# Kernel tuning notes

Measured on AMD Instinct MI355X. Metric: run time of the kernel, lower is better.

The kernel has to match this reference:

```python
import jax, jax.numpy as jnp
import numpy as np
import math

B, L, D, H = 2, 2048, 1024, 16
HD = D // H  # 64
SYNC_THRESHOLD = -0.7
LN_EPS = 1e-12


def setup_inputs() -> dict:
    key = jax.random.key(0)
    ks = jax.random.split(key, 12)
    s = 0.02
    return {
        "hidden_states": jax.random.normal(ks[0], (B, L, D), dtype=jnp.float32),
        "attention_mask": jnp.zeros((B, 1, 1, L), dtype=jnp.float32),
        "phi": jax.random.normal(ks[1], (B, L, H), dtype=jnp.float32),
        "Wq": jax.random.normal(ks[2], (D, D), dtype=jnp.float32) * s,
        "bq": jnp.zeros((D,), dtype=jnp.float32),
        "Wk": jax.random.normal(ks[3], (D, D), dtype=jnp.float32) * s,
        "bk": jnp.zeros((D,), dtype=jnp.float32),
        "Wv": jax.random.normal(ks[4], (D, D), dtype=jnp.float32) * s,
        "bv": jnp.zeros((D,), dtype=jnp.float32),
        "Wo": jax.random.normal(ks[5], (D, D), dtype=jnp.float32) * s,
        "bo": jnp.zeros((D,), dtype=jnp.float32),
        "ln_g": jnp.ones((D,), dtype=jnp.float32),
        "ln_b": jnp.zeros((D,), dtype=jnp.float32),
    }


def _shape(x):  # [B,L,D] -> [B,H,L,HD]
    return x.reshape(B, L, H, HD).transpose(0, 2, 1, 3)


def _rotate_half(x):
    x1, x2 = jnp.split(x, 2, axis=-1)
    return jnp.concatenate([-x2, x1], axis=-1)


def reference(hidden_states, attention_mask, phi, Wq, bq, Wk, bk, Wv, bv, Wo, bo, ln_g, ln_b):
    residual = hidden_states
    q = _shape(hidden_states @ Wq.T + bq)
    k = _shape(hidden_states @ Wk.T + bk)
    v = _shape(hidden_states @ Wv.T + bv)

    # phase per (batch, head, token): [B,H,L,1]; constant across head_dim,
    # so cos/sin of the concatenated phase are the same scalar per token/head.
    p = jnp.transpose(phi, (0, 2, 1))[..., None]
    cos_p = jnp.cos(p)
    sin_p = jnp.sin(p)
    q_rot = q * cos_p + _rotate_half(q) * sin_p
    k_rot = k * cos_p + _rotate_half(k) * sin_p

    scores = jnp.einsum("bhqd,bhkd->bhqk", q_rot, k_rot) / math.sqrt(HD)

    # data-dependent sync mask: mask pairs whose phase difference is anti-synced
    delta_phi = p - jnp.swapaxes(p, -1, -2)           # [B,H,L,L]
    eye = jnp.eye(L, dtype=bool)[None, None]          # [1,1,L,L]
    sync_mask = (jnp.cos(delta_phi) < SYNC_THRESHOLD) & ~eye
    scores = jnp.where(sync_mask, -1e9, scores)
    scores = scores + attention_mask

    # all-masked edge case: zero diagonal score so softmax attends to self
    row_max = jnp.max(scores, axis=-1, keepdims=True)
    all_masked = row_max <= -1e8
    scores = jnp.where(all_masked & eye, 0.0, scores)

    probs = jax.nn.softmax(scores, axis=-1)
    ctx = jnp.einsum("bhqk,bhkd->bhqd", probs, v)
    ctx = ctx.transpose(0, 2, 1, 3).reshape(B, L, D)

    out = ctx @ Wo.T + bo
    x = out + residual
    mean = jnp.mean(x, axis=-1, keepdims=True)
    var = jnp.var(x, axis=-1, keepdims=True)
    return (x - mean) / jnp.sqrt(var + LN_EPS) * ln_g + ln_b
```

## Files before the change

### kernel.cpp

```cpp
#include <hip/hip_runtime.h>
#include <cmath>

#define BB 2
#define LL 2048
#define DD 1024
#define HH 16
#define HDD 64

typedef _Float16 v8h __attribute__((ext_vector_type(8)));
typedef _Float16 v4h __attribute__((ext_vector_type(4)));
typedef _Float16 v2h __attribute__((ext_vector_type(2)));
typedef float v4f __attribute__((ext_vector_type(4)));

#define LOG2E 1.44269504089f
#define NEGB  (-1.442695e9f)

#define GLD(gp, lp)                                                        \
  __builtin_amdgcn_global_load_lds(                                        \
      (const __attribute__((address_space(1))) void*)(gp),                 \
      (__attribute__((address_space(3))) void*)(lp), 16, 0, 0)

__global__ __launch_bounds__(256) void prep(
    const float* __restrict__ hs, const float* __restrict__ wq,
    const float* __restrict__ wk, const float* __restrict__ wv,
    const float* __restrict__ wo, const float* __restrict__ phi,
    const float* __restrict__ amk, _Float16* __restrict__ hsh,
    _Float16* __restrict__ wqkvh, _Float16* __restrict__ woh,
    unsigned* __restrict__ csh2, float* __restrict__ aml2)
{
  const int i = blockIdx.x * 256 + threadIdx.x;
  if (i < 2097152) {
    const float* s;
    _Float16* d;
    if (i < 1048576)      { s = hs + (size_t)i * 4;            d = hsh + (size_t)i * 4; }
    else if (i < 1310720) { int j = i - 1048576; s = wq + (size_t)j * 4; d = wqkvh + (size_t)j * 4; }
    else if (i < 1572864) { int j = i - 1310720; s = wk + (size_t)j * 4; d = wqkvh + 1048576 + (size_t)j * 4; }
    else if (i < 1835008) { int j = i - 1572864; s = wv + (size_t)j * 4; d = wqkvh + 2097152 + (size_t)j * 4; }
    else                  { int j = i - 1835008; s = wo + (size_t)j * 4; d = woh + (size_t)j * 4; }
    float4 v = *(const float4*)s;
    v4h o;
    o[0] = (_Float16)v.x; o[1] = (_Float16)v.y;
    o[2] = (_Float16)v.z; o[3] = (_Float16)v.w;
    *(v4h*)d = o;
  } else {
    const int o = i - 2097152;
    if (o < BB * LL) aml2[o] = amk[o] * LOG2E;
    const int l = o & 2047;
    const int h = (o >> 11) & 15;
    const int b = o >> 15;
    const float ph = phi[(b * 2048 + l) * 16 + h];
    v2h cs;
    cs[0] = (_Float16)cosf(ph);
    cs[1] = (_Float16)sinf(ph);
    csh2[o] = __builtin_bit_cast(unsigned, cs);
  }
}

__device__ __forceinline__ void gemm_loop(
    const _Float16* __restrict__ A, const _Float16* __restrict__ W, const int K,
    const int m0, const int n0, const int tid, const int wave, const int lane,
    _Float16* As, _Float16* Bs, v4f acc[4][4])
{
  const int quad = lane >> 4;
  const int ql = lane & 15;
  const int wm = (wave >> 1) * 64;
  const int wn = (wave & 1) * 64;
  const int srow = tid >> 2;
  const int skof = (tid & 3) * 8;
  const _Float16* Ap = A + (size_t)(m0 + srow) * K + skof;
  const _Float16* Wp = W + (size_t)(n0 + srow) * K + skof;
  const size_t rstep = (size_t)64 * K;
  for (int k0 = 0; k0 < K; k0 += 32) {
    __syncthreads();
    GLD(Ap + k0,         As + tid * 8);
    GLD(Ap + rstep + k0, As + 2048 + tid * 8);
    GLD(Wp + k0,         Bs + tid * 8);
    GLD(Wp + rstep + k0, Bs + 2048 + tid * 8);
    __syncthreads();
    v8h af[4], bf[4];
#pragma unroll
    for (int mt = 0; mt < 4; ++mt)
      af[mt] = *(const v8h*)&As[(wm + mt * 16 + ql) * 32 + quad * 8];
#pragma unroll
    for (int nt = 0; nt < 4; ++nt)
      bf[nt] = *(const v8h*)&Bs[(wn + nt * 16 + ql) * 32 + quad * 8];
#pragma unroll
    for (int mt = 0; mt < 4; ++mt)
#pragma unroll
      for (int nt = 0; nt < 4; ++nt)
        acc[mt][nt] = __builtin_amdgcn_mfma_f32_16x16x32_f16(
            af[mt], bf[nt], acc[mt][nt], 0, 0, 0);
  }
}

__global__ __launch_bounds__(256) void gemm_qkv(
    const _Float16* __restrict__ A, const _Float16* __restrict__ W,
    const float* __restrict__ bqp, const float* __restrict__ bkp,
    const float* __restrict__ bvp, const unsigned* __restrict__ csh2,
    _Float16* __restrict__ qh, _Float16* __restrict__ kh,
    _Float16* __restrict__ vt2)
{
  __shared__ _Float16 As[128 * 32];
  __shared__ _Float16 Bs[128 * 32];
  const int tid = threadIdx.x, lane = tid & 63, wave = tid >> 6;
  const int quad = lane >> 4, ql = lane & 15;
  const int bid0 = blockIdx.y * 24 + blockIdx.x;
  const int bid  = (bid0 & 7) * 96 + (bid0 >> 3);
  const int m0 = (bid / 24) * 128, n0 = (bid % 24) * 128;
  v4f acc[4][4];
#pragma unroll
  for (int mt = 0; mt < 4; ++mt)
#pragma unroll
    for (int nt = 0; nt < 4; ++nt) acc[mt][nt] = (v4f){0.f, 0.f, 0.f, 0.f};
  gemm_loop(A, W, DD, m0, n0, tid, wave, lane, As, Bs, acc);

  const int buf = n0 >> 10;
  const int col0 = (n0 & 1023) + (wave & 1) * 64;
  const int hh = col0 >> 6;
  const int mr0 = m0 + (wave >> 1) * 64;

  if (buf == 2) {
    float bb4[4];
#pragma unroll
    for (int nt = 0; nt < 4; ++nt) bb4[nt] = bvp[col0 + nt * 16 + ql];
#pragma unroll
    for (int mt = 0; mt < 4; ++mt) {
      const int row = mr0 + mt * 16 + quad * 4;
      const int b_ = row >> 11;
      const int l = row & 2047;
      _Float16* dst = vt2 + ((size_t)(b_ * 16 + hh) * 32 + (l >> 6)) * 4096 +
                      ((l >> 2) & 15) * 256;
#pragma unroll
      for (int nt = 0; nt < 4; ++nt) {
        const int d = nt * 16 + ql;
        v4h o4;
#pragma unroll
        for (int r = 0; r < 4; ++r) o4[r] = (_Float16)(acc[mt][nt][r] + bb4[nt]);
        *(v4h*)&dst[d * 4] = o4;
      }
    }
  } else {
    const float scl = (buf == 0) ? 0.125f * LOG2E : 1.0f;
    _Float16* outp = (buf == 0) ? qh : kh;
    const float* bias = (buf == 0) ? bqp : bkp;
    float bb4[4];
#pragma unroll
    for (int nt = 0; nt < 4; ++nt) bb4[nt] = bias[col0 + nt * 16 + ql];
#pragma unroll
    for (int mt = 0; mt < 4; ++mt)
#pragma unroll
      for (int r = 0; r < 4; ++r) {
        const int row = mr0 + mt * 16 + quad * 4 + r;
        const int b_ = row >> 11;
        const int l = row & 2047;
        const v2h c2 = __builtin_bit_cast(
            v2h, csh2[(b_ * 16 + hh) * 2048 + l]);
        const float c = (float)c2[0], s = (float)c2[1];
        _Float16* orow = outp + (size_t)row * DD + col0 + ql;
#pragma unroll
        for (int pp = 0; pp < 2; ++pp) {
          const float a0 = acc[mt][pp][r] + bb4[pp];
          const float a1 = acc[mt][pp + 2][r] + bb4[pp + 2];
          orow[pp * 16]        = (_Float16)((a0 * c - a1 * s) * scl);
          orow[(pp + 2) * 16]  = (_Float16)((a1 * c + a0 * s) * scl);
        }
      }
  }
}

__global__ __launch_bounds__(256) void gemm_o(
    const _Float16* __restrict__ A, const _Float16* __restrict__ W,
    const float* __restrict__ bo, const float* __restrict__ res,
    float* __restrict__ out)
{
  __shared__ _Float16 As[128 * 32];
  __shared__ _Float16 Bs[64 * 32];
  const int tid = threadIdx.x, lane = tid & 63, wave = tid >> 6;
  const int quad = lane >> 4, ql = lane & 15;
  const int bid0 = blockIdx.y * 16 + blockIdx.x;
  const int bid  = (bid0 & 7) * 64 + (bid0 >> 3);
  const int m0 = (bid / 16) * 128, n0 = (bid % 16) * 64;
  v4f acc[4][2];
#pragma unroll
  for (int mt = 0; mt < 4; ++mt)
#pragma unroll
    for (int nt = 0; nt < 2; ++nt) acc[mt][nt] = (v4f){0.f, 0.f, 0.f, 0.f};
  const int wm = (wave >> 1) * 64;
  const int wn = (wave & 1) * 32;
  const int srow = tid >> 2;
  const int skof = (tid & 3) * 8;
  const _Float16* Ap = A + (size_t)(m0 + srow) * DD + skof;
  const _Float16* Wp = W + (size_t)(n0 + srow) * DD + skof;
  const size_t rstep = (size_t)64 * DD;
  for (int k0 = 0; k0 < DD; k0 += 32) {
    __syncthreads();
    GLD(Ap + k0,         As + tid * 8);
    GLD(Ap + rstep + k0, As + 2048 + tid * 8);
    GLD(Wp + k0,         Bs + tid * 8);
    __syncthreads();
    v8h af[4], bf[2];
#pragma unroll
    for (int mt = 0; mt < 4; ++mt)
      af[mt] = *(const v8h*)&As[(wm + mt * 16 + ql) * 32 + quad * 8];
#pragma unroll
    for (int nt = 0; nt < 2; ++nt)
      bf[nt] = *(const v8h*)&Bs[(wn + nt * 16 + ql) * 32 + quad * 8];
#pragma unroll
    for (int mt = 0; mt < 4; ++mt)
#pragma unroll
      for (int nt = 0; nt < 2; ++nt)
        acc[mt][nt] = __builtin_amdgcn_mfma_f32_16x16x32_f16(
            af[mt], bf[nt], acc[mt][nt], 0, 0, 0);
  }
#pragma unroll
  for (int nt = 0; nt < 2; ++nt) {
    const int col = n0 + wn + nt * 16 + ql;
    const float bb = bo[col];
#pragma unroll
    for (int mt = 0; mt < 4; ++mt)
#pragma unroll
      for (int r = 0; r < 4; ++r) {
        const int row = m0 + wm + mt * 16 + quad * 4 + r;
        const size_t ix = (size_t)row * DD + col;
        out[ix] = acc[mt][nt][r] + bb + res[ix];
      }
  }
}

__global__ __launch_bounds__(256, 2) void attn_db(
    const _Float16* __restrict__ Q, const _Float16* __restrict__ K,
    const _Float16* __restrict__ VT2, const unsigned* __restrict__ csh2,
    const float* __restrict__ aml2, _Float16* __restrict__ ctx)
{
  __shared__ _Float16 Kt[2][4096];
  __shared__ _Float16 Vt[2][4096];
  __shared__ float amL[LL];

  const int tid  = threadIdx.x;
  const int lane = tid & 63;
  const int wave = tid >> 6;
  const int quad = lane >> 4;
  const int ql   = lane & 15;
  const int bid  = blockIdx.x;
  const int bh = bid & 31;
  const int qt = bid >> 5;
  const int h  = bh & 15;
  const int b  = bh >> 4;
  const int q0w = qt * 128 + wave * 32;
  const int csb = bh * LL;

  {
    const float* amb = aml2 + b * LL;
    for (int i = tid; i < LL; i += 256) amL[i] = amb[i];
  }

  v8h qf0[2], qf1[2];
  v4h bq0, bq1;
  {
    const _Float16* qp = Q + ((size_t)(b * LL + q0w + ql)) * DD + h * 64 + quad * 8;
    qf0[0] = *(const v8h*)qp;
    qf0[1] = *(const v8h*)(qp + 32);
    const v2h c2 = __builtin_bit_cast(v2h, csh2[csb + q0w + ql]);
    v4h t = (v4h){0, 0, 0, 0};
    if (quad == 0) { t[0] = c2[0]; t[1] = c2[1]; }
    bq0 = t;
  }
  {
    const _Float16* qp = Q + ((size_t)(b * LL + q0w + 16 + ql)) * DD + h * 64 + quad * 8;
    qf1[0] = *(const v8h*)qp;
    qf1[1] = *(const v8h*)(qp + 32);
    const v2h c2 = __builtin_bit_cast(v2h, csh2[csb + q0w + 16 + ql]);
    v4h t = (v4h){0, 0, 0, 0};
    if (quad == 0) { t[0] = c2[0]; t[1] = c2[1]; }
    bq1 = t;
  }
  const v4h ones = (v4h){(_Float16)1.f, (_Float16)1.f,
                         (_Float16)1.f, (_Float16)1.f};

  v4f o0[4], o1[4];
#pragma unroll
  for (int nt = 0; nt < 4; ++nt) {
    o0[nt] = (v4f){0.f, 0.f, 0.f, 0.f};
    o1[nt] = (v4f){0.f, 0.f, 0.f, 0.f};
  }
  v4f lacc0 = (v4f){0.f, 0.f, 0.f, 0.f};
  v4f lacc1 = (v4f){0.f, 0.f, 0.f, 0.f};

  const _Float16* Kb   = K + (size_t)(b * LL) * DD + h * 64;
  const _Float16* VTb2 = VT2 + (size_t)bh * 131072;
  const unsigned* csk = csh2 + csb;

  const int srow = tid >> 3;
  const int kch  = (tid & 7) ^ (srow & 7);

  {
    const size_t kg = (size_t)srow * 1024 + kch * 8;
    GLD(Kb + kg,             &Kt[0][tid * 8]);
    GLD(Kb + kg + 32 * 1024, &Kt[0][2048 + tid * 8]);
    GLD(VTb2 + tid * 8,          &Vt[0][tid * 8]);
    GLD(VTb2 + 2048 + tid * 8,   &Vt[0][2048 + tid * 8]);
  }
  unsigned cs_cur[4], cs_nxt[4];
#pragma unroll
  for (int c = 0; c < 4; ++c) cs_cur[c] = csk[c * 16 + ql];
  __syncthreads();

  for (int tt = 0; tt < 16; ++tt) {
#pragma unroll
    for (int u = 0; u < 2; ++u) {
      const int t = tt * 2 + u;
      const int k0 = t * 64;
      if (t < 31) {
        const int k1 = k0 + 64;
        const size_t kg = (size_t)(k1 + srow) * 1024 + kch * 8;
        GLD(Kb + kg,             &Kt[u ^ 1][tid * 8]);
        GLD(Kb + kg + 32 * 1024, &Kt[u ^ 1][2048 + tid * 8]);
        const _Float16* vsrc = VTb2 + (size_t)(t + 1) * 4096;
        GLD(vsrc + tid * 8,        &Vt[u ^ 1][tid * 8]);
        GLD(vsrc + 2048 + tid * 8, &Vt[u ^ 1][2048 + tid * 8]);
#pragma unroll
        for (int c = 0; c < 4; ++c) cs_nxt[c] = csk[k1 + c * 16 + ql];
      }
      const _Float16* KtB = Kt[u];
      const _Float16* VtB = Vt[u];

      v4f st0[4], st1[4], dd0[4], dd1[4];
#pragma unroll
      for (int c = 0; c < 4; ++c) {
        const int row = c * 16 + ql;
        const int sw = row & 7;
        v8h a0 = *(const v8h*)&KtB[row * 64 + ((quad ^ sw) << 3)];
        v8h a1 = *(const v8h*)&KtB[row * 64 + (((quad + 4) ^ sw) << 3)];
        v4f z0 = (v4f){0.f, 0.f, 0.f, 0.f};
        z0 = __builtin_amdgcn_mfma_f32_16x16x32_f16(a0, qf0[0], z0, 0, 0, 0);
        z0 = __builtin_amdgcn_mfma_f32_16x16x32_f16(a1, qf0[1], z0, 0, 0, 0);
        st0[c] = z0;
        v4f z1 = (v4f){0.f, 0.f, 0.f, 0.f};
        z1 = __builtin_amdgcn_mfma_f32_16x16x32_f16(a0, qf1[0], z1, 0, 0, 0);
        z1 = __builtin_amdgcn_mfma_f32_16x16x32_f16(a1, qf1[1], z1, 0, 0, 0);
        st1[c] = z1;
        const v2h c2 = __builtin_bit_cast(v2h, cs_cur[c]);
        v4h a = (v4h){0, 0, 0, 0};
        if (quad == 0) { a[0] = c2[0]; a[1] = c2[1]; }
        dd0[c] = __builtin_amdgcn_mfma_f32_16x16x16f16(
            a, bq0, (v4f){0.f, 0.f, 0.f, 0.f}, 0, 0, 0);
        dd1[c] = __builtin_amdgcn_mfma_f32_16x16x16f16(
            a, bq1, (v4f){0.f, 0.f, 0.f, 0.f}, 0, 0, 0);
      }

      v4h pf0[4], pf1[4];
#pragma unroll
      for (int c = 0; c < 4; ++c) {
        const v4f am4 = *(const v4f*)&amL[k0 + c * 16 + quad * 4];
        float p0[4], p1[4];
#pragma unroll
        for (int r = 0; r < 4; ++r) {
          p0[r] = __builtin_amdgcn_exp2f(
              ((dd0[c][r] < -0.7f) ? NEGB : st0[c][r]) + am4[r]);
          p1[r] = __builtin_amdgcn_exp2f(
              ((dd1[c][r] < -0.7f) ? NEGB : st1[c][r]) + am4[r]);
        }
        const unsigned a01 = __builtin_bit_cast(
            unsigned, __builtin_amdgcn_cvt_pkrtz(p0[0], p0[1]));
        const unsigned a23 = __builtin_bit_cast(
            unsigned, __builtin_amdgcn_cvt_pkrtz(p0[2], p0[3]));
        pf0[c] = __builtin_bit_cast(v4h, make_uint2(a01, a23));
        const unsigned b01 = __builtin_bit_cast(
            unsigned, __builtin_amdgcn_cvt_pkrtz(p1[0], p1[1]));
        const unsigned b23 = __builtin_bit_cast(
            unsigned, __builtin_amdgcn_cvt_pkrtz(p1[2], p1[3]));
        pf1[c] = __builtin_bit_cast(v4h, make_uint2(b01, b23));
      }

      __builtin_amdgcn_s_setprio(1);
#pragma unroll
      for (int c = 0; c < 4; ++c) {
        lacc0 = __builtin_amdgcn_mfma_f32_16x16x16f16(pf0[c], ones, lacc0, 0, 0, 0);
        lacc1 = __builtin_amdgcn_mfma_f32_16x16x16f16(pf1[c], ones, lacc1, 0, 0, 0);
#pragma unroll
        for (int nt = 0; nt < 4; ++nt) {
          const v4h vv = *(const v4h*)&VtB[((c * 4 + quad) * 64 +
                                            nt * 16 + ql) * 4];
          o0[nt] = __builtin_amdgcn_mfma_f32_16x16x16f16(pf0[c], vv, o0[nt], 0, 0, 0);
          o1[nt] = __builtin_amdgcn_mfma_f32_16x16x16f16(pf1[c], vv, o1[nt], 0, 0, 0);
        }
      }
      __builtin_amdgcn_s_setprio(0);
#pragma unroll
      for (int c = 0; c < 4; ++c) cs_cur[c] = cs_nxt[c];
      __syncthreads();
    }
  }

#pragma unroll
  for (int g = 0; g < 2; ++g) {
    const v4f* op = g ? o1 : o0;
    const v4f la = g ? lacc1 : lacc0;
#pragma unroll
    for (int r = 0; r < 4; ++r) {
      const int q = q0w + g * 16 + quad * 4 + r;
      const float lr = la[r];
      const size_t ob = (size_t)(b * LL + q) * DD + h * 64 + ql;
      if (lr <= 0.f) {
        const _Float16* vsrc = VTb2 + (q >> 6) * 4096 +
                               ((q >> 2) & 15) * 256 + (q & 3);
#pragma unroll
        for (int nt = 0; nt < 4; ++nt)
          ctx[ob + nt * 16] = vsrc[(nt * 16 + ql) * 4];
      } else {
        const float inv = 1.f / lr;
        ctx[ob + 0]  = (_Float16)(op[0][r] * inv);
        ctx[ob + 16] = (_Float16)(op[1][r] * inv);
        ctx[ob + 32] = (_Float16)(op[2][r] * inv);
        ctx[ob + 48] = (_Float16)(op[3][r] * inv);
      }
    }
  }
}

__global__ __launch_bounds__(256) void layernorm(
    const float* __restrict__ x, const float* __restrict__ g,
    const float* __restrict__ bta, float* __restrict__ out)
{
  __shared__ float red[8];
  const int row = blockIdx.x;
  const int tid = threadIdx.x;
  const float4 vv = ((const float4*)(x + (size_t)row * DD))[tid];
  float lsum = vv.x + vv.y + vv.z + vv.w;
  float lsq  = vv.x * vv.x + vv.y * vv.y + vv.z * vv.z + vv.w * vv.w;
#pragma unroll
  for (int off = 32; off > 0; off >>= 1) {
    lsum += __shfl_down(lsum, off, 64);
    lsq  += __shfl_down(lsq,  off, 64);
  }
  const int wid = tid >> 6;
  if ((tid & 63) == 0) { red[wid] = lsum; red[wid + 4] = lsq; }
  __syncthreads();
  const float tsum = red[0] + red[1] + red[2] + red[3];
  const float tsq  = red[4] + red[5] + red[6] + red[7];
  const float mean = tsum * (1.f / DD);
  const float var  = tsq * (1.f / DD) - mean * mean;
  const float inv  = rsqrtf(var + 1e-12f);
  const float4 gg = ((const float4*)g)[tid];
  const float4 bb = ((const float4*)bta)[tid];
  float4 oo;
  oo.x = (vv.x - mean) * inv * gg.x + bb.x;
  oo.y = (vv.y - mean) * inv * gg.y + bb.y;
  oo.z = (vv.z - mean) * inv * gg.z + bb.z;
  oo.w = (vv.w - mean) * inv * gg.w + bb.w;
  ((float4*)(out + (size_t)row * DD))[tid] = oo;
}

extern "C" void kernel_launch(void* const* d_in, const int* in_sizes, int n_in,
                              void* d_out, int out_size, void* d_ws, size_t ws_size,
                              hipStream_t stream)
{
  const float* hs  = (const float*)d_in[0];
  const float* amk = (const float*)d_in[1];
  const float* phi = (const float*)d_in[2];
  const float* Wq  = (const float*)d_in[3];
  const float* bq  = (const float*)d_in[4];
  const float* Wk  = (const float*)d_in[5];
  const float* bk  = (const float*)d_in[6];
  const float* Wv  = (const float*)d_in[7];
  const float* bv  = (const float*)d_in[8];
  const float* Wo  = (const float*)d_in[9];
  const float* bo  = (const float*)d_in[10];
  const float* lng = (const float*)d_in[11];
  const float* lnb = (const float*)d_in[12];
  float* out = (float*)d_out;

  const size_t SZ = (size_t)BB * LL * DD;
  _Float16* hsh   = (_Float16*)d_ws;
  _Float16* qh    = hsh + SZ;
  _Float16* kh    = qh + SZ;
  _Float16* vt2   = kh + SZ;
  _Float16* ctxh  = vt2 + SZ;
  _Float16* wqkvh = ctxh + SZ;
  _Float16* woh   = wqkvh + 3 * (size_t)DD * DD;
  float* xb    = (float*)(woh + (size_t)DD * DD);
  unsigned* csh2 = (unsigned*)(xb + SZ);
  float* aml2 = (float*)(csh2 + (size_t)BB * HH * LL);

  prep<<<8448, 256, 0, stream>>>(hs, Wq, Wk, Wv, Wo, phi, amk,
                                 hsh, wqkvh, woh, csh2, aml2);
  gemm_qkv<<<dim3(24, 32), 256, 0, stream>>>(hsh, wqkvh, bq, bk, bv, csh2,
                                             qh, kh, vt2);
  attn_db<<<512, 256, 0, stream>>>(qh, kh, vt2, csh2, aml2, ctxh);
  gemm_o<<<dim3(16, 32), 256, 0, stream>>>(ctxh, woh, bo, hs, xb);
  layernorm<<<BB * LL, 256, 0, stream>>>(xb, lng, lnb, out);
}
```

Before: 230.7 us.

## Fuse output projection with LayerNorm via atomic row stats and grid sync

Merges the output GEMM and the LayerNorm kernel into one cooperative kernel. Each block adds bias and residual in registers, then atomically accumulates per-row sum and sum-of-squares into global buffers that prep zeroes. After a grid-wide sync it normalizes in place and writes the final output. This removes the fp32 intermediate round trip and one kernel launch, at the cost of a grid barrier, atomic contention, and the requirement that all 512 blocks be co-resident.

After: 348.4 us. +51.0%, slower.

```diff
diff --git a/kernel.cpp b/kernel.cpp
--- a/kernel.cpp
+++ b/kernel.cpp
@@ -1,5 +1,8 @@
 #include <hip/hip_runtime.h>
+#include <hip/hip_cooperative_groups.h>
 #include <cmath>
+
+namespace cg = cooperative_groups;
 
 #define BB 2
 #define LL 2048
@@ -26,7 +29,8 @@
     const float* __restrict__ wo, const float* __restrict__ phi,
     const float* __restrict__ amk, _Float16* __restrict__ hsh,
     _Float16* __restrict__ wqkvh, _Float16* __restrict__ woh,
-    unsigned* __restrict__ csh2, float* __restrict__ aml2)
+    unsigned* __restrict__ csh2, float* __restrict__ aml2,
+    float* __restrict__ rsum, float* __restrict__ rsq)
 {
   const int i = blockIdx.x * 256 + threadIdx.x;
   if (i < 2097152) {
@@ -42,7 +46,7 @@
     o[0] = (_Float16)v.x; o[1] = (_Float16)v.y;
     o[2] = (_Float16)v.z; o[3] = (_Float16)v.w;
     *(v4h*)d = o;
-  } else {
+  } else if (i < 2162688) {
     const int o = i - 2097152;
     if (o < BB * LL) aml2[o] = amk[o] * LOG2E;
     const int l = o & 2047;
@@ -53,6 +57,10 @@
     cs[0] = (_Float16)cosf(ph);
     cs[1] = (_Float16)sinf(ph);
     csh2[o] = __builtin_bit_cast(unsigned, cs);
+  } else {
+    const int z = i - 2162688;
+    rsum[z] = 0.f;
+    rsq[z]  = 0.f;
   }
 }
 
@@ -168,9 +176,11 @@
   }
 }
 
-__global__ __launch_bounds__(256) void gemm_o(
+__global__ __launch_bounds__(256, 2) void gemm_o_ln(
     const _Float16* __restrict__ A, const _Float16* __restrict__ W,
     const float* __restrict__ bo, const float* __restrict__ res,
+    const float* __restrict__ g, const float* __restrict__ bta,
+    float* __restrict__ rsum, float* __restrict__ rsq,
     float* __restrict__ out)
 {
   __shared__ _Float16 As[128 * 32];
@@ -212,19 +222,61 @@
         acc[mt][nt] = __builtin_amdgcn_mfma_f32_16x16x32_f16(
             af[mt], bf[nt], acc[mt][nt], 0, 0, 0);
   }
-#pragma unroll
-  for (int nt = 0; nt < 2; ++nt) {
-    const int col = n0 + wn + nt * 16 + ql;
-    const float bb = bo[col];
-#pragma unroll
-    for (int mt = 0; mt < 4; ++mt)
-#pragma unroll
-      for (int r = 0; r < 4; ++r) {
+
+  float bb[2];
+#pragma unroll
+  for (int nt = 0; nt < 2; ++nt) bb[nt] = bo[n0 + wn + nt * 16 + ql];
+#pragma unroll
+  for (int mt = 0; mt < 4; ++mt)
+#pragma unroll
+    for (int r = 0; r < 4; ++r) {
+      const int row = m0 + wm + mt * 16 + quad * 4 + r;
+#pragma unroll
+      for (int nt = 0; nt < 2; ++nt) {
+        const int col = n0 + wn + nt * 16 + ql;
+        acc[mt][nt][r] += bb[nt] + res[(size_t)row * DD + col];
+      }
+    }
+#pragma unroll
+  for (int mt = 0; mt < 4; ++mt)
+#pragma unroll
+    for (int r = 0; r < 4; ++r) {
+      const float a = acc[mt][0][r], b = acc[mt][1][r];
+      float s = a + b;
+      float q2 = a * a + b * b;
+#pragma unroll
+      for (int off = 1; off < 16; off <<= 1) {
+        s  += __shfl_xor(s,  off, 64);
+        q2 += __shfl_xor(q2, off, 64);
+      }
+      if (ql == 0) {
         const int row = m0 + wm + mt * 16 + quad * 4 + r;
-        const size_t ix = (size_t)row * DD + col;
-        out[ix] = acc[mt][nt][r] + bb + res[ix];
-      }
-  }
+        atomicAdd(&rsum[row], s);
+        atomicAdd(&rsq[row],  q2);
+      }
+    }
+  __threadfence();
+  cg::this_grid().sync();
+
+#pragma unroll
+  for (int mt = 0; mt < 4; ++mt)
+#pragma unroll
+    for (int r = 0; r < 4; ++r) {
+      const int row = m0 + wm + mt * 16 + quad * 4 + r;
+      const float ts = __hip_atomic_load(&rsum[row], __ATOMIC_RELAXED,
+                                         __HIP_MEMORY_SCOPE_AGENT);
+      const float tq = __hip_atomic_load(&rsq[row], __ATOMIC_RELAXED,
+                                         __HIP_MEMORY_SCOPE_AGENT);
+      const float mean = ts * (1.f / DD);
+      const float var  = tq * (1.f / DD) - mean * mean;
+      const float inv  = rsqrtf(var + 1e-12f);
+#pragma unroll
+      for (int nt = 0; nt < 2; ++nt) {
+        const int col = n0 + wn + nt * 16 + ql;
+        out[(size_t)row * DD + col] =
+            (acc[mt][nt][r] - mean) * inv * g[col] + bta[col];
+      }
+    }
 }
 
 __global__ __launch_bounds__(256, 2) void attn_db(
@@ -418,39 +470,6 @@
   }
 }
 
-__global__ __launch_bounds__(256) void layernorm(
-    const float* __restrict__ x, const float* __restrict__ g,
-    const float* __restrict__ bta, float* __restrict__ out)
-{
-  __shared__ float red[8];
-  const int row = blockIdx.x;
-  const int tid = threadIdx.x;
-  const float4 vv = ((const float4*)(x + (size_t)row * DD))[tid];
-  float lsum = vv.x + vv.y + vv.z + vv.w;
-  float lsq  = vv.x * vv.x + vv.y * vv.y + vv.z * vv.z + vv.w * vv.w;
-#pragma unroll
-  for (int off = 32; off > 0; off >>= 1) {
-    lsum += __shfl_down(lsum, off, 64);
-    lsq  += __shfl_down(lsq,  off, 64);
-  }
-  const int wid = tid >> 6;
-  if ((tid & 63) == 0) { red[wid] = lsum; red[wid + 4] = lsq; }
-  __syncthreads();
-  const float tsum = red[0] + red[1] + red[2] + red[3];
-  const float tsq  = red[4] + red[5] + red[6] + red[7];
-  const float mean = tsum * (1.f / DD);
-  const float var  = tsq * (1.f / DD) - mean * mean;
-  const float inv  = rsqrtf(var + 1e-12f);
-  const float4 gg = ((const float4*)g)[tid];
-  const float4 bb = ((const float4*)bta)[tid];
-  float4 oo;
-  oo.x = (vv.x - mean) * inv * gg.x + bb.x;
-  oo.y = (vv.y - mean) * inv * gg.y + bb.y;
-  oo.z = (vv.z - mean) * inv * gg.z + bb.z;
-  oo.w = (vv.w - mean) * inv * gg.w + bb.w;
-  ((float4*)(out + (size_t)row * DD))[tid] = oo;
-}
-
 extern "C" void kernel_launch(void* const* d_in, const int* in_sizes, int n_in,
                               void* d_out, int out_size, void* d_ws, size_t ws_size,
                               hipStream_t stream)
@@ -478,15 +497,23 @@
   _Float16* ctxh  = vt2 + SZ;
   _Float16* wqkvh = ctxh + SZ;
   _Float16* woh   = wqkvh + 3 * (size_t)DD * DD;
-  float* xb    = (float*)(woh + (size_t)DD * DD);
-  unsigned* csh2 = (unsigned*)(xb + SZ);
+  unsigned* csh2 = (unsigned*)(woh + (size_t)DD * DD);
   float* aml2 = (float*)(csh2 + (size_t)BB * HH * LL);
-
-  prep<<<8448, 256, 0, stream>>>(hs, Wq, Wk, Wv, Wo, phi, amk,
-                                 hsh, wqkvh, woh, csh2, aml2);
+  float* rsum = aml2 + (size_t)BB * LL;
+  float* rsq  = rsum + (size_t)BB * LL;
+
+  prep<<<8464, 256, 0, stream>>>(hs, Wq, Wk, Wv, Wo, phi, amk,
+                                 hsh, wqkvh, woh, csh2, aml2, rsum, rsq);
   gemm_qkv<<<dim3(24, 32), 256, 0, stream>>>(hsh, wqkvh, bq, bk, bv, csh2,
                                              qh, kh, vt2);
   attn_db<<<512, 256, 0, stream>>>(qh, kh, vt2, csh2, aml2, ctxh);
-  gemm_o<<<dim3(16, 32), 256, 0, stream>>>(ctxh, woh, bo, hs, xb);
-  layernorm<<<BB * LL, 256, 0, stream>>>(xb, lng, lnb, out);
+  {
+    const _Float16* a_ = ctxh;
+    const _Float16* w_ = woh;
+    void* args[] = {(void*)&a_, (void*)&w_, (void*)&bo, (void*)&hs,
+                    (void*)&lng, (void*)&lnb, (void*)&rsum, (void*)&rsq,
+                    (void*)&out};
+    hipLaunchCooperativeKernel((void*)gemm_o_ln, dim3(16, 32), dim3(256),
+                               args, 0, stream);
+  }
 }
```

## Split attention key range across wave pairs and merge partial results in LDS

Applied to the files above, without the earlier changes.

Doubles the attention block to 512 threads, with each pair of waves sharing the same 32 queries while each wave handles half of the key sequence, so every wave runs 16 key tiles instead of 32. K/V tiles for both halves are double-buffered in separate LDS regions. At the end, the second-half waves write their partial output and row-sum accumulators to LDS and the first-half waves add them before normalizing and storing. This shortens the serial key loop per wave and raises the wave count to hide latency, at the cost of more LDS, a final reduction step, and possible occupancy limits from the larger block. The merge is a plain add, which is only valid because the kernel appears to use a fixed softmax offset rather than a running max.

After: 298.9 us. 29.6% more time.

```diff
diff --git a/kernel.cpp b/kernel.cpp
--- a/kernel.cpp
+++ b/kernel.cpp
@@ -227,13 +227,13 @@
   }
 }
 
-__global__ __launch_bounds__(256, 2) void attn_db(
+__global__ __launch_bounds__(512, 4) void attn_db(
     const _Float16* __restrict__ Q, const _Float16* __restrict__ K,
     const _Float16* __restrict__ VT2, const unsigned* __restrict__ csh2,
     const float* __restrict__ aml2, _Float16* __restrict__ ctx)
 {
-  __shared__ _Float16 Kt[2][4096];
-  __shared__ _Float16 Vt[2][4096];
+  __shared__ _Float16 Kt[2][2][4096];
+  __shared__ _Float16 Vt[2][2][4096];
   __shared__ float amL[LL];
 
   const int tid  = threadIdx.x;
@@ -246,12 +246,15 @@
   const int qt = bid >> 5;
   const int h  = bh & 15;
   const int b  = bh >> 4;
-  const int q0w = qt * 128 + wave * 32;
+  const int pair = wave >> 1;
+  const int kh2  = wave & 1;
+  const int q0w = qt * 128 + pair * 32;
   const int csb = bh * LL;
+  const int kbase = kh2 << 10;
 
   {
     const float* amb = aml2 + b * LL;
-    for (int i = tid; i < LL; i += 256) amL[i] = amb[i];
+    for (int i = tid; i < LL; i += 512) amL[i] = amb[i];
   }
 
   v8h qf0[2], qf1[2];
@@ -292,37 +295,38 @@
 
   const int srow = tid >> 3;
   const int kch  = (tid & 7) ^ (srow & 7);
+  const size_t kgb = (size_t)srow * 1024 + kch * 8;
 
   {
-    const size_t kg = (size_t)srow * 1024 + kch * 8;
-    GLD(Kb + kg,             &Kt[0][tid * 8]);
-    GLD(Kb + kg + 32 * 1024, &Kt[0][2048 + tid * 8]);
-    GLD(VTb2 + tid * 8,          &Vt[0][tid * 8]);
-    GLD(VTb2 + 2048 + tid * 8,   &Vt[0][2048 + tid * 8]);
+    GLD(Kb + kgb,                          &Kt[0][0][tid * 8]);
+    GLD(Kb + kgb + (size_t)1024 * 1024,    &Kt[1][0][tid * 8]);
+    GLD(VTb2 + tid * 8,                    &Vt[0][0][tid * 8]);
+    GLD(VTb2 + 65536 + tid * 8,            &Vt[1][0][tid * 8]);
   }
   unsigned cs_cur[4], cs_nxt[4];
 #pragma unroll
-  for (int c = 0; c < 4; ++c) cs_cur[c] = csk[c * 16 + ql];
+  for (int c = 0; c < 4; ++c) cs_cur[c] = csk[kbase + c * 16 + ql];
   __syncthreads();
 
-  for (int tt = 0; tt < 16; ++tt) {
+  for (int tt = 0; tt < 8; ++tt) {
 #pragma unroll
     for (int u = 0; u < 2; ++u) {
-      const int t = tt * 2 + u;
-      const int k0 = t * 64;
-      if (t < 31) {
-        const int k1 = k0 + 64;
-        const size_t kg = (size_t)(k1 + srow) * 1024 + kch * 8;
-        GLD(Kb + kg,             &Kt[u ^ 1][tid * 8]);
-        GLD(Kb + kg + 32 * 1024, &Kt[u ^ 1][2048 + tid * 8]);
-        const _Float16* vsrc = VTb2 + (size_t)(t + 1) * 4096;
-        GLD(vsrc + tid * 8,        &Vt[u ^ 1][tid * 8]);
-        GLD(vsrc + 2048 + tid * 8, &Vt[u ^ 1][2048 + tid * 8]);
-#pragma unroll
-        for (int c = 0; c < 4; ++c) cs_nxt[c] = csk[k1 + c * 16 + ql];
-      }
-      const _Float16* KtB = Kt[u];
-      const _Float16* VtB = Vt[u];
+      const int s = tt * 2 + u;
+      const int k0 = kbase + s * 64;
+      if (s < 15) {
+        const int t1 = s + 1;
+        const size_t kg0 = kgb + (size_t)(t1 * 64) * 1024;
+        GLD(Kb + kg0,                        &Kt[0][u ^ 1][tid * 8]);
+        GLD(Kb + kg0 + (size_t)1024 * 1024,  &Kt[1][u ^ 1][tid * 8]);
+        const _Float16* vsrc = VTb2 + (size_t)t1 * 4096;
+        GLD(vsrc + tid * 8,          &Vt[0][u ^ 1][tid * 8]);
+        GLD(vsrc + 65536 + tid * 8,  &Vt[1][u ^ 1][tid * 8]);
+#pragma unroll
+        for (int c = 0; c < 4; ++c)
+          cs_nxt[c] = csk[kbase + t1 * 64 + c * 16 + ql];
+      }
+      const _Float16* KtB = Kt[kh2][u];
+      const _Float16* VtB = Vt[kh2][u];
 
       v4f st0[4], st1[4], dd0[4], dd1[4];
 #pragma unroll
@@ -392,27 +396,51 @@
     }
   }
 
-#pragma unroll
-  for (int g = 0; g < 2; ++g) {
-    const v4f* op = g ? o1 : o0;
-    const v4f la = g ? lacc1 : lacc0;
-#pragma unroll
-    for (int r = 0; r < 4; ++r) {
-      const int q = q0w + g * 16 + quad * 4 + r;
-      const float lr = la[r];
-      const size_t ob = (size_t)(b * LL + q) * DD + h * 64 + ql;
-      if (lr <= 0.f) {
-        const _Float16* vsrc = VTb2 + (q >> 6) * 4096 +
-                               ((q >> 2) & 15) * 256 + (q & 3);
-#pragma unroll
-        for (int nt = 0; nt < 4; ++nt)
-          ctx[ob + nt * 16] = vsrc[(nt * 16 + ql) * 4];
-      } else {
-        const float inv = 1.f / lr;
-        ctx[ob + 0]  = (_Float16)(op[0][r] * inv);
-        ctx[ob + 16] = (_Float16)(op[1][r] * inv);
-        ctx[ob + 32] = (_Float16)(op[2][r] * inv);
-        ctx[ob + 48] = (_Float16)(op[3][r] * inv);
+  v4f* shO = (v4f*)&Kt[0][0][0];
+  v4f* shL = (v4f*)&Vt[0][0][0];
+  if (kh2 == 1) {
+    const int ob = (pair * 64 + lane) * 8;
+#pragma unroll
+    for (int nt = 0; nt < 4; ++nt) {
+      shO[ob + nt]     = o0[nt];
+      shO[ob + 4 + nt] = o1[nt];
+    }
+    shL[(pair * 64 + lane) * 2]     = lacc0;
+    shL[(pair * 64 + lane) * 2 + 1] = lacc1;
+  }
+  __syncthreads();
+  if (kh2 == 0) {
+    const int ob = (pair * 64 + lane) * 8;
+#pragma unroll
+    for (int nt = 0; nt < 4; ++nt) {
+      o0[nt] += shO[ob + nt];
+      o1[nt] += shO[ob + 4 + nt];
+    }
+    lacc0 += shL[(pair * 64 + lane) * 2];
+    lacc1 += shL[(pair * 64 + lane) * 2 + 1];
+
+#pragma unroll
+    for (int g = 0; g < 2; ++g) {
+      const v4f* op = g ? o1 : o0;
+      const v4f la = g ? lacc1 : lacc0;
+#pragma unroll
+      for (int r = 0; r < 4; ++r) {
+        const int q = q0w + g * 16 + quad * 4 + r;
+        const float lr = la[r];
+        const size_t ob2 = (size_t)(b * LL + q) * DD + h * 64 + ql;
+        if (lr <= 0.f) {
+          const _Float16* vsrc = VTb2 + (q >> 6) * 4096 +
+                                 ((q >> 2) & 15) * 256 + (q & 3);
+#pragma unroll
+          for (int nt = 0; nt < 4; ++nt)
+            ctx[ob2 + nt * 16] = vsrc[(nt * 16 + ql) * 4];
+        } else {
+          const float inv = 1.f / lr;
+          ctx[ob2 + 0]  = (_Float16)(op[0][r] * inv);
+          ctx[ob2 + 16] = (_Float16)(op[1][r] * inv);
+          ctx[ob2 + 32] = (_Float16)(op[2][r] * inv);
+          ctx[ob2 + 48] = (_Float16)(op[3][r] * inv);
+        }
       }
     }
   }
@@ -486,7 +514,7 @@
                                  hsh, wqkvh, woh, csh2, aml2);
   gemm_qkv<<<dim3(24, 32), 256, 0, stream>>>(hsh, wqkvh, bq, bk, bv, csh2,
                                              qh, kh, vt2);
-  attn_db<<<512, 256, 0, stream>>>(qh, kh, vt2, csh2, aml2, ctxh);
+  attn_db<<<512, 512, 0, stream>>>(qh, kh, vt2, csh2, aml2, ctxh);
   gemm_o<<<dim3(16, 32), 256, 0, stream>>>(ctxh, woh, bo, hs, xb);
   layernorm<<<BB * LL, 256, 0, stream>>>(xb, lng, lnb, out);
 }
```
